# Performance work log

Measured on AMD Instinct MI355X. Metric: run time of the kernel, lower is better.

The kernel has to match this reference:

```python
import jax, jax.numpy as jnp
import numpy as np

B, N, C = 4, 2048, 320
H, D = 5, 64            # heads, dim_head
INNER = H * D           # 320


def setup_inputs() -> dict:
    key = jax.random.key(0)
    ks = jax.random.split(key, 7)
    x = jax.random.normal(ks[0], (B, N, C), dtype=jnp.float32)
    edge = jax.random.uniform(ks[1], (B, N, 1), dtype=jnp.float32)
    s = 1.0 / np.sqrt(C)
    Wq = jax.random.normal(ks[2], (C, INNER), dtype=jnp.float32) * s
    Wk = jax.random.normal(ks[3], (C, INNER), dtype=jnp.float32) * s
    Wv = jax.random.normal(ks[4], (C, INNER), dtype=jnp.float32) * s
    Wo = jax.random.normal(ks[5], (INNER, C), dtype=jnp.float32) * (1.0 / np.sqrt(INNER))
    bo = jnp.zeros((C,), dtype=jnp.float32)
    return {"x": x, "edge": edge, "Wq": Wq, "Wk": Wk, "Wv": Wv, "Wo": Wo, "bo": bo}


def _split_heads(t):
    # 'b n (h d) -> (b h) n d'  (batch-major, head-minor)
    b, n, _ = t.shape
    return t.reshape(b, n, H, D).transpose(0, 2, 1, 3).reshape(b * H, n, D)


def reference(x, edge, Wq, Wk, Wv, Wo, bo):
    scale = D ** -0.5
    q = _split_heads(x @ Wq).astype(jnp.float32)   # (B*H, N, D)
    k = _split_heads(x @ Wk).astype(jnp.float32)
    v = _split_heads(x @ Wv)

    sim = jnp.einsum('bid,bjd->bij', q, k) * scale  # (B*H, N, N)

    # torch: edge.repeat(h, 1, 1) -> batch-minor tiling; index i uses edge[i % B]
    edge_rep = jnp.tile(edge, (H, 1, 1))            # (H*B, N, 1)
    edge_matrix = edge_rep * edge_rep.transpose(0, 2, 1)  # outer product (H*B, N, N)

    sim = jax.nn.softmax(sim * edge_matrix, axis=-1)
    out = jnp.einsum('bij,bjd->bid', sim, v)        # (B*H, N, D)

    # '(b h) n d -> b n (h d)'
    out = out.reshape(B, H, N, D).transpose(0, 2, 1, 3).reshape(B, N, INNER)
    return out @ Wo + bo
```

## Files before the change

kernel.cpp:

```cpp
#include <hip/hip_runtime.h>
#include <hip/hip_bf16.h>
#include <math.h>


typedef short bf16x8 __attribute__((ext_vector_type(8)));
typedef float f32x4 __attribute__((ext_vector_type(4)));

static __device__ __forceinline__ ushort f2bf(float f) {
  union { float f; unsigned u; } v; v.f = f;
  unsigned r = (v.u + 0x7fffu + ((v.u >> 16) & 1u)) >> 16;
  return (ushort)r;
}
static __device__ __forceinline__ float fexp2(float x) {
#if __has_builtin(__builtin_amdgcn_exp2f)
  return __builtin_amdgcn_exp2f(x);
#else
  return exp2f(x);
#endif
}
static __device__ __forceinline__ f32x4 mfma32(bf16x8 a, bf16x8 b, f32x4 c) {
  return __builtin_amdgcn_mfma_f32_16x16x32_bf16(a, b, c, 0, 0, 0);
}

__global__ __launch_bounds__(256) void xcvt_kernel(
    const float* __restrict__ x, ushort* __restrict__ xb)
{
  const int t = threadIdx.x;
  const int mt2 = blockIdx.x;
  const int kc = blockIdx.y * 2 + (t >> 7);
  const int f = (t & 127) * 4;
  const int qq = f >> 7, mm = (f >> 3) & 15, e0 = f & 7;
  float4 v = *reinterpret_cast<const float4*>(
      x + (size_t)(mt2 * 16 + mm) * 320 + kc * 32 + qq * 8 + e0);
  ushort4 o = { f2bf(v.x), f2bf(v.y), f2bf(v.z), f2bf(v.w) };
  *reinterpret_cast<ushort4*>(xb + (size_t)(mt2 * 10 + kc) * 512 + f) = o;
}

__global__ __launch_bounds__(256) void wtrans_kernel(
    const float* __restrict__ Wq, const float* __restrict__ Wk,
    const float* __restrict__ Wv, const float* __restrict__ Wo,
    ushort* __restrict__ wt)
{
  const int z = blockIdx.z;
  const float* W = z == 0 ? Wq : z == 1 ? Wk : z == 2 ? Wv : Wo;
  const int nt2 = blockIdx.x, kc = blockIdx.y;
  const int f = threadIdx.x * 2;
  const int qq = f >> 7, nn = (f >> 3) & 15, e0 = f & 7;
  const int k = kc * 32 + qq * 8 + e0, n = nt2 * 16 + nn;
  float v0 = W[(size_t)k * 320 + n];
  float v1 = W[(size_t)(k + 1) * 320 + n];
  ushort2 o = { f2bf(v0), f2bf(v1) };
  *reinterpret_cast<ushort2*>(
      wt + (size_t)z * 102400 + (size_t)(nt2 * 10 + kc) * 512 + f) = o;
}

__global__ __launch_bounds__(256, 4) void qkv_gemm(
    const ushort* __restrict__ xb, const float* __restrict__ edge,
    const ushort* __restrict__ wt,
    ushort* __restrict__ qp, ushort* __restrict__ kS, ushort* __restrict__ vS)
{
  const int mt = blockIdx.x, h = blockIdx.y, z = blockIdx.z;
  const int wave = threadIdx.x >> 6, lane = threadIdx.x & 63;
  const int m16 = lane & 15, quad = lane >> 4;
  const int m0 = mt * 64 + wave * 16;
  const ushort* atile = xb + (size_t)(mt * 4 + wave) * 10 * 512 + lane * 8;
  const ushort* btile = wt + (size_t)z * 102400 + (size_t)(h * 4) * 10 * 512 + lane * 8;

  f32x4 acc[4];
#pragma unroll
  for (int ns = 0; ns < 4; ++ns) acc[ns] = (f32x4){0.f, 0.f, 0.f, 0.f};

#pragma unroll
  for (int kc = 0; kc < 10; ++kc) {
    bf16x8 af = *reinterpret_cast<const bf16x8*>(atile + kc * 512);
#pragma unroll
    for (int ns = 0; ns < 4; ++ns) {
      bf16x8 bf = *reinterpret_cast<const bf16x8*>(btile + (ns * 10 + kc) * 512);
      acc[ns] = mfma32(af, bf, acc[ns]);
    }
  }

  const float QSCALE = 0.18033688011112042f;
  const int mrow = m0 + quad * 4;
  const int b = mrow >> 11;
  const int n = mrow & 2047;
  const int bh = b * 5 + h;
  if (z == 2) {
#pragma unroll
    for (int ns = 0; ns < 4; ++ns) {
      ushort4 o = { f2bf(acc[ns][0]), f2bf(acc[ns][1]),
                    f2bf(acc[ns][2]), f2bf(acc[ns][3]) };
      size_t addr = (size_t)bh * 131072 + (size_t)ns * 32768 +
                    (size_t)(mt & 31) * 1024 + (wave >> 1) * 512 +
                    (quad * 16 + m16) * 8 + (wave & 1) * 4;
      *reinterpret_cast<ushort4*>(vS + addr) = o;
    }
  } else if (z == 1) {
    const float* eb = edge + (size_t)((b + h) & 3) * 2048;
    const size_t base = (size_t)bh * 131072 + (size_t)((mt & 31) * 4 + wave) * 1024;
#pragma unroll
    for (int ns = 0; ns < 4; ++ns) {
      int d = ns * 16 + m16;
      size_t a0 = base + (ns >> 1) * 512 +
                  (((ns & 1) * 2 + (m16 >> 3)) * 16 + quad * 4) * 8 + (m16 & 7);
#pragma unroll
      for (int r = 0; r < 4; ++r)
        kS[a0 + (size_t)r * 8] = f2bf(acc[ns][r] * eb[n + r]);
    }
  } else {
    const float* eb = edge + (size_t)((b + h) & 3) * 2048;
    float e[4];
#pragma unroll
    for (int r = 0; r < 4; ++r) e[r] = eb[n + r] * QSCALE;
    ushort* dst = qp + ((size_t)bh * 2048 + n) * 64;
#pragma unroll
    for (int ns = 0; ns < 4; ++ns) {
      int d = ns * 16 + m16;
#pragma unroll
      for (int r = 0; r < 4; ++r)
        dst[(size_t)r * 64 + d] = f2bf(acc[ns][r] * e[r]);
    }
  }
}

__global__ __launch_bounds__(256, 4) void attn_kernel(
    const ushort* __restrict__ qp, const ushort* __restrict__ kS,
    const ushort* __restrict__ vS, ushort* __restrict__ ao)
{
  __shared__ f32x4 lo[3][8][64];
  __shared__ float lrs[4][2][16];
  const int qt = blockIdx.x, bh = blockIdx.y;
  const int b = bh / 5, h = bh % 5;
  const int wave = threadIdx.x >> 6, lane = threadIdx.x & 63;
  const int m16 = lane & 15, quad = lane >> 4;
  const int q0 = qt * 32;

  bf16x8 qf[2][2];
#pragma unroll
  for (int qs = 0; qs < 2; ++qs) {
    const ushort* qrow = qp + ((size_t)bh * 2048 + q0 + qs * 16 + m16) * 64;
    qf[qs][0] = *reinterpret_cast<const bf16x8*>(qrow + quad * 8);
    qf[qs][1] = *reinterpret_cast<const bf16x8*>(qrow + 32 + quad * 8);
  }
  const ushort* kb_p = kS + (size_t)bh * 131072 + lane * 8;
  const ushort* vb_p = vS + (size_t)bh * 131072 + lane * 8;

  f32x4 oacc[2][4], rsacc[2];
#pragma unroll
  for (int qs = 0; qs < 2; ++qs) {
    rsacc[qs] = (f32x4){0.f, 0.f, 0.f, 0.f};
    for (int dt = 0; dt < 4; ++dt) oacc[qs][dt] = (f32x4){0.f, 0.f, 0.f, 0.f};
  }
  const bf16x8 ones8 = {(short)16256, (short)16256, (short)16256, (short)16256,
                        (short)16256, (short)16256, (short)16256, (short)16256};

  for (int i = 0; i < 8; ++i) {
    const int jb = i * 4 + wave;
#pragma unroll
    for (int kb = 0; kb < 2; ++kb) {
      bf16x8 kf[2][2];
#pragma unroll
      for (int s = 0; s < 2; ++s)
#pragma unroll
        for (int hf = 0; hf < 2; ++hf)
          kf[s][hf] = *reinterpret_cast<const bf16x8*>(
              kb_p + (size_t)(jb * 4 + kb * 2 + s) * 1024 + hf * 512);
      bf16x8 vf[4];
#pragma unroll
      for (int dt = 0; dt < 4; ++dt)
        vf[dt] = *reinterpret_cast<const bf16x8*>(
            vb_p + (size_t)dt * 32768 + (size_t)jb * 1024 + kb * 512);
#pragma unroll
      for (int qs = 0; qs < 2; ++qs) {
        f32x4 st0 = (f32x4){0.f, 0.f, 0.f, 0.f};
        f32x4 st1 = (f32x4){0.f, 0.f, 0.f, 0.f};
        st0 = mfma32(kf[0][0], qf[qs][0], st0);
        st0 = mfma32(kf[0][1], qf[qs][1], st0);
        st1 = mfma32(kf[1][0], qf[qs][0], st1);
        st1 = mfma32(kf[1][1], qf[qs][1], st1);
        unsigned b0 = __float_as_uint(fexp2(st0[0]));
        unsigned b1 = __float_as_uint(fexp2(st0[1]));
        unsigned b2 = __float_as_uint(fexp2(st0[2]));
        unsigned b3 = __float_as_uint(fexp2(st0[3]));
        unsigned b4 = __float_as_uint(fexp2(st1[0]));
        unsigned b5 = __float_as_uint(fexp2(st1[1]));
        unsigned b6 = __float_as_uint(fexp2(st1[2]));
        unsigned b7 = __float_as_uint(fexp2(st1[3]));
        union { unsigned u[4]; bf16x8 v; } pk;
        pk.u[0] = __builtin_amdgcn_perm(b1, b0, 0x07060302u);
        pk.u[1] = __builtin_amdgcn_perm(b3, b2, 0x07060302u);
        pk.u[2] = __builtin_amdgcn_perm(b5, b4, 0x07060302u);
        pk.u[3] = __builtin_amdgcn_perm(b7, b6, 0x07060302u);
        rsacc[qs] = mfma32(ones8, pk.v, rsacc[qs]);
#pragma unroll
        for (int dt = 0; dt < 4; ++dt)
          oacc[qs][dt] = mfma32(vf[dt], pk.v, oacc[qs][dt]);
      }
    }
  }

  if (wave > 0) {
#pragma unroll
    for (int qs = 0; qs < 2; ++qs)
#pragma unroll
      for (int dt = 0; dt < 4; ++dt)
        lo[wave - 1][qs * 4 + dt][lane] = oacc[qs][dt];
  }
  if (quad == 0) {
    lrs[wave][0][m16] = rsacc[0][0];
    lrs[wave][1][m16] = rsacc[1][0];
  }
  __syncthreads();
  if (wave == 0) {
#pragma unroll
    for (int qs = 0; qs < 2; ++qs) {
      float inv = 1.0f / (lrs[0][qs][m16] + lrs[1][qs][m16] +
                          lrs[2][qs][m16] + lrs[3][qs][m16]);
      const int mt2 = b * 128 + qt * 2 + qs;
#pragma unroll
      for (int dt = 0; dt < 4; ++dt) {
        f32x4 a = oacc[qs][dt];
        a += lo[0][qs * 4 + dt][lane];
        a += lo[1][qs * 4 + dt][lane];
        a += lo[2][qs * 4 + dt][lane];
        unsigned r0 = f2bf(a[0] * inv), r1 = f2bf(a[1] * inv);
        unsigned r2 = f2bf(a[2] * inv), r3 = f2bf(a[3] * inv);
        uint2 w;
        w.x = r0 | (r1 << 16);
        w.y = r2 | (r3 << 16);
        size_t addr = (size_t)(mt2 * 10 + h * 2 + (dt >> 1)) * 512 +
                      ((((dt & 1) * 2 + (quad >> 1)) * 16 + m16)) * 8 +
                      (quad & 1) * 4;
        *reinterpret_cast<uint2*>(ao + addr) = w;
      }
    }
  }
}

__global__ __launch_bounds__(256, 4) void oproj_gemm(
    const ushort* __restrict__ ao, const ushort* __restrict__ wt,
    const float* __restrict__ bo, float* __restrict__ out)
{
  const int mt = blockIdx.x, ct = blockIdx.y;
  const int wave = threadIdx.x >> 6, lane = threadIdx.x & 63;
  const int m16 = lane & 15, quad = lane >> 4;
  const int m0 = mt * 64 + wave * 16;
  const int n0 = ct * 64;
  const ushort* atile = ao + (size_t)(mt * 4 + wave) * 10 * 512 + lane * 8;
  const ushort* btile = wt + (size_t)3 * 102400 + (size_t)(ct * 4) * 10 * 512 + lane * 8;

  f32x4 acc[4];
#pragma unroll
  for (int ns = 0; ns < 4; ++ns) acc[ns] = (f32x4){0.f, 0.f, 0.f, 0.f};

#pragma unroll
  for (int kc = 0; kc < 10; ++kc) {
    bf16x8 af = *reinterpret_cast<const bf16x8*>(atile + kc * 512);
#pragma unroll
    for (int ns = 0; ns < 4; ++ns) {
      bf16x8 bf = *reinterpret_cast<const bf16x8*>(btile + (ns * 10 + kc) * 512);
      acc[ns] = mfma32(af, bf, acc[ns]);
    }
  }

  float bb[4];
#pragma unroll
  for (int ns = 0; ns < 4; ++ns) bb[ns] = bo[n0 + ns * 16 + m16];
  const int mrow = m0 + quad * 4;
#pragma unroll
  for (int ns = 0; ns < 4; ++ns)
#pragma unroll
    for (int r = 0; r < 4; ++r)
      out[(size_t)(mrow + r) * 320 + n0 + ns * 16 + m16] = acc[ns][r] + bb[ns];
}

extern "C" void kernel_launch(void* const* d_in, const int* in_sizes, int n_in,
                              void* d_out, int out_size, void* d_ws, size_t ws_size,
                              hipStream_t stream) {
  const float* x    = (const float*)d_in[0];
  const float* edge = (const float*)d_in[1];
  const float* Wq   = (const float*)d_in[2];
  const float* Wk   = (const float*)d_in[3];
  const float* Wv   = (const float*)d_in[4];
  const float* Wo   = (const float*)d_in[5];
  const float* bo   = (const float*)d_in[6];
  float* out = (float*)d_out;

  ushort* xb = (ushort*)d_ws;
  ushort* wt = xb + (size_t)8192 * 320;
  ushort* qp = wt + (size_t)4 * 320 * 320;
  ushort* kS = qp + (size_t)20 * 2048 * 64;
  ushort* vS = kS + (size_t)20 * 2048 * 64;
  ushort* ao = vS + (size_t)20 * 2048 * 64;

  xcvt_kernel<<<dim3(512, 5), 256, 0, stream>>>(x, xb);
  wtrans_kernel<<<dim3(20, 10, 4), 256, 0, stream>>>(Wq, Wk, Wv, Wo, wt);
  qkv_gemm<<<dim3(128, 5, 3), 256, 0, stream>>>(xb, edge, wt, qp, kS, vS);
  attn_kernel<<<dim3(64, 20), 256, 0, stream>>>(qp, kS, vS, ao);
  oproj_gemm<<<dim3(128, 5), 256, 0, stream>>>(ao, wt, bo, out);
}
```

Baseline: 142.2 us.

## Fuse QKV projections per block and double query tile with K/V prefetch

The QKV GEMM now computes Q, K and V in one block, so each A-tile load is reused three times and the grid's z dimension goes away. The attention kernel processes 64 query rows per block instead of 32, halving the number of K/V reloads across the grid. It also double-buffers the K/V fragment loads so the next unit's loads overlap the current unit's MFMA work. The cost is higher register pressure (launch bounds lowered to 2 blocks per CU), more LDS for the cross-wave reduction, and fewer attention blocks (640), which may leave some CUs underused.

```diff
diff --git a/kernel.cpp b/kernel.cpp
--- a/kernel.cpp
+++ b/kernel.cpp
@@ -59,25 +59,30 @@
     const ushort* __restrict__ wt,
     ushort* __restrict__ qp, ushort* __restrict__ kS, ushort* __restrict__ vS)
 {
-  const int mt = blockIdx.x, h = blockIdx.y, z = blockIdx.z;
+  const int mt = blockIdx.x, h = blockIdx.y;
   const int wave = threadIdx.x >> 6, lane = threadIdx.x & 63;
   const int m16 = lane & 15, quad = lane >> 4;
   const int m0 = mt * 64 + wave * 16;
   const ushort* atile = xb + (size_t)(mt * 4 + wave) * 10 * 512 + lane * 8;
-  const ushort* btile = wt + (size_t)z * 102400 + (size_t)(h * 4) * 10 * 512 + lane * 8;
-
-  f32x4 acc[4];
-#pragma unroll
-  for (int ns = 0; ns < 4; ++ns) acc[ns] = (f32x4){0.f, 0.f, 0.f, 0.f};
+  const ushort* btile = wt + (size_t)(h * 4) * 10 * 512 + lane * 8;
+
+  f32x4 acc[3][4];
+#pragma unroll
+  for (int z = 0; z < 3; ++z)
+#pragma unroll
+    for (int ns = 0; ns < 4; ++ns) acc[z][ns] = (f32x4){0.f, 0.f, 0.f, 0.f};
 
 #pragma unroll
   for (int kc = 0; kc < 10; ++kc) {
     bf16x8 af = *reinterpret_cast<const bf16x8*>(atile + kc * 512);
 #pragma unroll
-    for (int ns = 0; ns < 4; ++ns) {
-      bf16x8 bf = *reinterpret_cast<const bf16x8*>(btile + (ns * 10 + kc) * 512);
-      acc[ns] = mfma32(af, bf, acc[ns]);
-    }
+    for (int z = 0; z < 3; ++z)
+#pragma unroll
+      for (int ns = 0; ns < 4; ++ns) {
+        bf16x8 bf = *reinterpret_cast<const bf16x8*>(
+            btile + (size_t)z * 102400 + (ns * 10 + kc) * 512);
+        acc[z][ns] = mfma32(af, bf, acc[z][ns]);
+      }
   }
 
   const float QSCALE = 0.18033688011112042f;
@@ -85,59 +90,60 @@
   const int b = mrow >> 11;
   const int n = mrow & 2047;
   const int bh = b * 5 + h;
-  if (z == 2) {
+  const float* eb = edge + (size_t)((b + h) & 3) * 2048;
+  float e[4];
+#pragma unroll
+  for (int r = 0; r < 4; ++r) e[r] = eb[n + r];
+
+  {
+    ushort* dst = qp + ((size_t)bh * 2048 + n) * 64;
 #pragma unroll
     for (int ns = 0; ns < 4; ++ns) {
-      ushort4 o = { f2bf(acc[ns][0]), f2bf(acc[ns][1]),
-                    f2bf(acc[ns][2]), f2bf(acc[ns][3]) };
+      int d = ns * 16 + m16;
+#pragma unroll
+      for (int r = 0; r < 4; ++r)
+        dst[(size_t)r * 64 + d] = f2bf(acc[0][ns][r] * e[r] * QSCALE);
+    }
+  }
+  {
+    const size_t base = (size_t)bh * 131072 + (size_t)((mt & 31) * 4 + wave) * 1024;
+#pragma unroll
+    for (int ns = 0; ns < 4; ++ns) {
+      size_t a0 = base + (ns >> 1) * 512 +
+                  (((ns & 1) * 2 + (m16 >> 3)) * 16 + quad * 4) * 8 + (m16 & 7);
+#pragma unroll
+      for (int r = 0; r < 4; ++r)
+        kS[a0 + (size_t)r * 8] = f2bf(acc[1][ns][r] * e[r]);
+    }
+  }
+  {
+#pragma unroll
+    for (int ns = 0; ns < 4; ++ns) {
+      ushort4 o = { f2bf(acc[2][ns][0]), f2bf(acc[2][ns][1]),
+                    f2bf(acc[2][ns][2]), f2bf(acc[2][ns][3]) };
       size_t addr = (size_t)bh * 131072 + (size_t)ns * 32768 +
                     (size_t)(mt & 31) * 1024 + (wave >> 1) * 512 +
                     (quad * 16 + m16) * 8 + (wave & 1) * 4;
       *reinterpret_cast<ushort4*>(vS + addr) = o;
     }
-  } else if (z == 1) {
-    const float* eb = edge + (size_t)((b + h) & 3) * 2048;
-    const size_t base = (size_t)bh * 131072 + (size_t)((mt & 31) * 4 + wave) * 1024;
-#pragma unroll
-    for (int ns = 0; ns < 4; ++ns) {
-      int d = ns * 16 + m16;
-      size_t a0 = base + (ns >> 1) * 512 +
-                  (((ns & 1) * 2 + (m16 >> 3)) * 16 + quad * 4) * 8 + (m16 & 7);
-#pragma unroll
-      for (int r = 0; r < 4; ++r)
-        kS[a0 + (size_t)r * 8] = f2bf(acc[ns][r] * eb[n + r]);
-    }
-  } else {
-    const float* eb = edge + (size_t)((b + h) & 3) * 2048;
-    float e[4];
-#pragma unroll
-    for (int r = 0; r < 4; ++r) e[r] = eb[n + r] * QSCALE;
-    ushort* dst = qp + ((size_t)bh * 2048 + n) * 64;
-#pragma unroll
-    for (int ns = 0; ns < 4; ++ns) {
-      int d = ns * 16 + m16;
-#pragma unroll
-      for (int r = 0; r < 4; ++r)
-        dst[(size_t)r * 64 + d] = f2bf(acc[ns][r] * e[r]);
-    }
-  }
-}
-
-__global__ __launch_bounds__(256, 4) void attn_kernel(
+  }
+}
+
+__global__ __launch_bounds__(256, 2) void attn_kernel(
     const ushort* __restrict__ qp, const ushort* __restrict__ kS,
     const ushort* __restrict__ vS, ushort* __restrict__ ao)
 {
-  __shared__ f32x4 lo[3][8][64];
-  __shared__ float lrs[4][2][16];
+  __shared__ f32x4 lo[3][16][64];
+  __shared__ float lrs[4][4][16];
   const int qt = blockIdx.x, bh = blockIdx.y;
   const int b = bh / 5, h = bh % 5;
   const int wave = threadIdx.x >> 6, lane = threadIdx.x & 63;
   const int m16 = lane & 15, quad = lane >> 4;
-  const int q0 = qt * 32;
-
-  bf16x8 qf[2][2];
-#pragma unroll
-  for (int qs = 0; qs < 2; ++qs) {
+  const int q0 = qt * 64;
+
+  bf16x8 qf[4][2];
+#pragma unroll
+  for (int qs = 0; qs < 4; ++qs) {
     const ushort* qrow = qp + ((size_t)bh * 2048 + q0 + qs * 16 + m16) * 64;
     qf[qs][0] = *reinterpret_cast<const bf16x8*>(qrow + quad * 8);
     qf[qs][1] = *reinterpret_cast<const bf16x8*>(qrow + 32 + quad * 8);
@@ -145,78 +151,86 @@
   const ushort* kb_p = kS + (size_t)bh * 131072 + lane * 8;
   const ushort* vb_p = vS + (size_t)bh * 131072 + lane * 8;
 
-  f32x4 oacc[2][4], rsacc[2];
-#pragma unroll
-  for (int qs = 0; qs < 2; ++qs) {
+  f32x4 oacc[4][4], rsacc[4];
+#pragma unroll
+  for (int qs = 0; qs < 4; ++qs) {
     rsacc[qs] = (f32x4){0.f, 0.f, 0.f, 0.f};
     for (int dt = 0; dt < 4; ++dt) oacc[qs][dt] = (f32x4){0.f, 0.f, 0.f, 0.f};
   }
   const bf16x8 ones8 = {(short)16256, (short)16256, (short)16256, (short)16256,
                         (short)16256, (short)16256, (short)16256, (short)16256};
 
-  for (int i = 0; i < 8; ++i) {
-    const int jb = i * 4 + wave;
-#pragma unroll
-    for (int kb = 0; kb < 2; ++kb) {
-      bf16x8 kf[2][2];
-#pragma unroll
-      for (int s = 0; s < 2; ++s)
-#pragma unroll
-        for (int hf = 0; hf < 2; ++hf)
-          kf[s][hf] = *reinterpret_cast<const bf16x8*>(
-              kb_p + (size_t)(jb * 4 + kb * 2 + s) * 1024 + hf * 512);
-      bf16x8 vf[4];
+  auto load_unit = [&](int u, bf16x8 kf[2][2], bf16x8 vf[4]) {
+    const int jb = (u >> 1) * 4 + wave, kb = u & 1;
+#pragma unroll
+    for (int s = 0; s < 2; ++s)
+#pragma unroll
+      for (int hf = 0; hf < 2; ++hf)
+        kf[s][hf] = *reinterpret_cast<const bf16x8*>(
+            kb_p + (size_t)(jb * 4 + kb * 2 + s) * 1024 + hf * 512);
+#pragma unroll
+    for (int dt = 0; dt < 4; ++dt)
+      vf[dt] = *reinterpret_cast<const bf16x8*>(
+          vb_p + (size_t)dt * 32768 + (size_t)jb * 1024 + kb * 512);
+  };
+  auto compute_unit = [&](bf16x8 kf[2][2], bf16x8 vf[4]) {
+#pragma unroll
+    for (int qs = 0; qs < 4; ++qs) {
+      f32x4 st0 = (f32x4){0.f, 0.f, 0.f, 0.f};
+      f32x4 st1 = (f32x4){0.f, 0.f, 0.f, 0.f};
+      st0 = mfma32(kf[0][0], qf[qs][0], st0);
+      st0 = mfma32(kf[0][1], qf[qs][1], st0);
+      st1 = mfma32(kf[1][0], qf[qs][0], st1);
+      st1 = mfma32(kf[1][1], qf[qs][1], st1);
+      unsigned b0 = __float_as_uint(fexp2(st0[0]));
+      unsigned b1 = __float_as_uint(fexp2(st0[1]));
+      unsigned b2 = __float_as_uint(fexp2(st0[2]));
+      unsigned b3 = __float_as_uint(fexp2(st0[3]));
+      unsigned b4 = __float_as_uint(fexp2(st1[0]));
+      unsigned b5 = __float_as_uint(fexp2(st1[1]));
+      unsigned b6 = __float_as_uint(fexp2(st1[2]));
+      unsigned b7 = __float_as_uint(fexp2(st1[3]));
+      union { unsigned u[4]; bf16x8 v; } pk;
+      pk.u[0] = __builtin_amdgcn_perm(b1, b0, 0x07060302u);
+      pk.u[1] = __builtin_amdgcn_perm(b3, b2, 0x07060302u);
+      pk.u[2] = __builtin_amdgcn_perm(b5, b4, 0x07060302u);
+      pk.u[3] = __builtin_amdgcn_perm(b7, b6, 0x07060302u);
+      rsacc[qs] = mfma32(ones8, pk.v, rsacc[qs]);
 #pragma unroll
       for (int dt = 0; dt < 4; ++dt)
-        vf[dt] = *reinterpret_cast<const bf16x8*>(
-            vb_p + (size_t)dt * 32768 + (size_t)jb * 1024 + kb * 512);
-#pragma unroll
-      for (int qs = 0; qs < 2; ++qs) {
-        f32x4 st0 = (f32x4){0.f, 0.f, 0.f, 0.f};
-        f32x4 st1 = (f32x4){0.f, 0.f, 0.f, 0.f};
-        st0 = mfma32(kf[0][0], qf[qs][0], st0);
-        st0 = mfma32(kf[0][1], qf[qs][1], st0);
-        st1 = mfma32(kf[1][0], qf[qs][0], st1);
-        st1 = mfma32(kf[1][1], qf[qs][1], st1);
-        unsigned b0 = __float_as_uint(fexp2(st0[0]));
-        unsigned b1 = __float_as_uint(fexp2(st0[1]));
-        unsigned b2 = __float_as_uint(fexp2(st0[2]));
-        unsigned b3 = __float_as_uint(fexp2(st0[3]));
-        unsigned b4 = __float_as_uint(fexp2(st1[0]));
-        unsigned b5 = __float_as_uint(fexp2(st1[1]));
-        unsigned b6 = __float_as_uint(fexp2(st1[2]));
-        unsigned b7 = __float_as_uint(fexp2(st1[3]));
-        union { unsigned u[4]; bf16x8 v; } pk;
-        pk.u[0] = __builtin_amdgcn_perm(b1, b0, 0x07060302u);
-        pk.u[1] = __builtin_amdgcn_perm(b3, b2, 0x07060302u);
-        pk.u[2] = __builtin_amdgcn_perm(b5, b4, 0x07060302u);
-        pk.u[3] = __builtin_amdgcn_perm(b7, b6, 0x07060302u);
-        rsacc[qs] = mfma32(ones8, pk.v, rsacc[qs]);
-#pragma unroll
-        for (int dt = 0; dt < 4; ++dt)
-          oacc[qs][dt] = mfma32(vf[dt], pk.v, oacc[qs][dt]);
-      }
-    }
+        oacc[qs][dt] = mfma32(vf[dt], pk.v, oacc[qs][dt]);
+    }
+  };
+
+  bf16x8 kA[2][2], vA[4], kB[2][2], vB[4];
+  load_unit(0, kA, vA);
+#pragma unroll
+  for (int u = 0; u < 16; u += 2) {
+    load_unit(u + 1, kB, vB);
+    compute_unit(kA, vA);
+    if (u + 2 < 16) load_unit(u + 2, kA, vA);
+    compute_unit(kB, vB);
   }
 
   if (wave > 0) {
 #pragma unroll
-    for (int qs = 0; qs < 2; ++qs)
+    for (int qs = 0; qs < 4; ++qs)
 #pragma unroll
       for (int dt = 0; dt < 4; ++dt)
         lo[wave - 1][qs * 4 + dt][lane] = oacc[qs][dt];
   }
   if (quad == 0) {
-    lrs[wave][0][m16] = rsacc[0][0];
-    lrs[wave][1][m16] = rsacc[1][0];
+#pragma unroll
+    for (int qs = 0; qs < 4; ++qs)
+      lrs[wave][qs][m16] = rsacc[qs][0];
   }
   __syncthreads();
   if (wave == 0) {
 #pragma unroll
-    for (int qs = 0; qs < 2; ++qs) {
+    for (int qs = 0; qs < 4; ++qs) {
       float inv = 1.0f / (lrs[0][qs][m16] + lrs[1][qs][m16] +
                           lrs[2][qs][m16] + lrs[3][qs][m16]);
-      const int mt2 = b * 128 + qt * 2 + qs;
+      const int mt2 = b * 128 + qt * 4 + qs;
 #pragma unroll
       for (int dt = 0; dt < 4; ++dt) {
         f32x4 a = oacc[qs][dt];
@@ -295,7 +309,7 @@
 
   xcvt_kernel<<<dim3(512, 5), 256, 0, stream>>>(x, xb);
   wtrans_kernel<<<dim3(20, 10, 4), 256, 0, stream>>>(Wq, Wk, Wv, Wo, wt);
-  qkv_gemm<<<dim3(128, 5, 3), 256, 0, stream>>>(xb, edge, wt, qp, kS, vS);
-  attn_kernel<<<dim3(64, 20), 256, 0, stream>>>(qp, kS, vS, ao);
+  qkv_gemm<<<dim3(128, 5), 256, 0, stream>>>(xb, edge, wt, qp, kS, vS);
+  attn_kernel<<<dim3(32, 20), 256, 0, stream>>>(qp, kS, vS, ao);
   oproj_gemm<<<dim3(128, 5), 256, 0, stream>>>(ao, wt, bo, out);
 }
```

Result: slower. 152.1 us (+7.0%).
